# Performance work log

Measured on AMD Instinct MI355X. Metric: run time of the kernel, lower is better.

Reference implementation:

```python
import jax, jax.numpy as jnp
import numpy as np

HEADS = 8
DIM_HEAD = 64
SCALE = DIM_HEAD ** -0.5


def setup_inputs() -> dict:
    key = jax.random.key(0)
    ks = jax.random.split(key, 6)
    b, dim, h, w = 8, 512, 64, 64
    ctx_dim, n = 768, 256
    inner = HEADS * DIM_HEAD  # 512
    x = jax.random.normal(ks[0], (b, dim, h, w), jnp.float32)
    context = jax.random.normal(ks[1], (b, n, ctx_dim), jnp.float32)
    # 1x1 convs / linear reduced to [out, in] matrices
    Wq = jax.random.normal(ks[2], (inner, dim), jnp.float32) * 0.02
    Wkv = jax.random.normal(ks[3], (2 * inner, ctx_dim), jnp.float32) * 0.02
    Wout = jax.random.normal(ks[4], (dim, inner), jnp.float32) * 0.02
    bout = jnp.zeros((dim,), jnp.float32)
    return {"x": x, "context": context, "Wq": Wq, "Wkv": Wkv, "Wout": Wout, "bout": bout}


def reference(x, context, Wq, Wkv, Wout, bout):
    b, c, h, w = x.shape
    # to_q: 1x1 conv (no bias) == per-pixel channel matmul
    q = jnp.einsum('bcxy,ec->bexy', x, Wq)              # [b, inner, h, w]
    # rearrange 'b (h d) x y -> b h (x y) d'
    q = q.reshape(b, HEADS, DIM_HEAD, h * w).transpose(0, 1, 3, 2)
    # to_kv: Linear(context_dim -> 2*inner, no bias)
    kv = jnp.einsum('bnc,ec->bne', context, Wkv)        # [b, n, 2*inner]
    k, v = jnp.split(kv, 2, axis=-1)
    # rearrange 'b n (h d) -> b h n d'
    n = context.shape[1]
    k = k.reshape(b, n, HEADS, DIM_HEAD).transpose(0, 2, 1, 3)
    v = v.reshape(b, n, HEADS, DIM_HEAD).transpose(0, 2, 1, 3)
    sim = jnp.einsum('bhid,bhjd->bhij', q, k) * SCALE   # [b, h, hw, n]
    attn = jax.nn.softmax(sim, axis=-1)
    out = jnp.einsum('bhij,bhjd->bhid', attn, v)        # [b, h, hw, d]
    # rearrange 'b h (x y) d -> b (h d) x y'
    out = out.transpose(0, 1, 3, 2).reshape(b, HEADS * DIM_HEAD, h, w)
    # to_out: 1x1 conv with bias, plus residual
    out = jnp.einsum('bexy,ce->bcxy', out, Wout) + bout[None, :, None, None]
    return out + x
```

## Files before the change

kernel.cpp:

```cpp
#include <hip/hip_runtime.h>

typedef unsigned short u16;
typedef __bf16 bf16x8 __attribute__((ext_vector_type(8)));
typedef __bf16 bf16x4 __attribute__((ext_vector_type(4)));
typedef float f32x4 __attribute__((ext_vector_type(4)));

__device__ __forceinline__ u16 f2bf(float f) {
  __bf16 h = (__bf16)f;
  return *(u16*)&h;
}

__device__ __forceinline__ f32x4 mfma16(bf16x8 a, bf16x8 b, f32x4 c) {
  return __builtin_amdgcn_mfma_f32_16x16x32_bf16(a, b, c, 0, 0, 0);
}

__device__ __forceinline__ void async16(void* lds, const void* g) {
  __builtin_amdgcn_global_load_lds(
      (const __attribute__((address_space(1))) unsigned int*)g,
      (__attribute__((address_space(3))) unsigned int*)lds, 16, 0, 0);
}

#define QSCALE 0.18033688011112042f

__global__ __launch_bounds__(256) void prep_transpose(
    const float* __restrict__ x, const float* __restrict__ Wq,
    const float* __restrict__ Wkv, const float* __restrict__ Wout,
    const float* __restrict__ ctx, u16* __restrict__ xT,
    u16* __restrict__ Wq_b, u16* __restrict__ Wkv_b,
    u16* __restrict__ Wout_b, u16* __restrict__ ctx_b) {
  __shared__ float tile[64][65];
  int bx = blockIdx.x;
  if (bx < 1024) {
    const long NWQ = 512L * 512, NWKV = 1024L * 768, NWOUT = 512L * 512,
               NCTX = 2048L * 768;
    const long total = NWQ + NWKV + NWOUT + NCTX;
    long stride = 1024L * 256;
    for (long i = (long)bx * 256 + threadIdx.x; i < total; i += stride) {
      long j = i;
      if (j < NWQ) { Wq_b[j] = f2bf(Wq[j] * QSCALE); continue; }
      j -= NWQ;
      if (j < NWKV) { Wkv_b[j] = f2bf(Wkv[j]); continue; }
      j -= NWKV;
      if (j < NWOUT) { Wout_b[j] = f2bf(Wout[j]); continue; }
      j -= NWOUT;
      ctx_b[j] = f2bf(ctx[j]);
    }
    return;
  }
  bx -= 1024;
  const int p0 = (bx & 63) * 64, c0 = ((bx >> 6) & 7) * 64, b = bx >> 9;
  const int tx = threadIdx.x & 63, ty = threadIdx.x >> 6;
  const float* xb = x + (long)b * (512L * 4096);
  #pragma unroll
  for (int i = ty; i < 64; i += 4)
    tile[i][tx] = xb[(long)(c0 + i) * 4096 + p0 + tx];
  __syncthreads();
  u16* xTb = xT + (long)b * (4096L * 512);
  #pragma unroll
  for (int i = ty; i < 64; i += 4)
    xTb[(long)(p0 + i) * 512 + c0 + tx] = f2bf(tile[tx][i]);
}

__global__ __launch_bounds__(256) void transpose_v(const u16* __restrict__ kv,
                                                   u16* __restrict__ vT) {
  __shared__ u16 tile[64][65];
  const int b = blockIdx.z, e0 = blockIdx.x * 64, n0 = blockIdx.y * 64;
  const int tx = threadIdx.x & 63, ty = threadIdx.x >> 6;
  #pragma unroll
  for (int i = ty; i < 64; i += 4)
    tile[i][tx] = kv[(long)(b * 256 + n0 + i) * 1024 + 512 + e0 + tx];
  __syncthreads();
  #pragma unroll
  for (int i = ty; i < 64; i += 4)
    vT[(long)b * (512L * 256) + (long)(e0 + i) * 256 + n0 + tx] = tile[tx][i];
}

__global__ __launch_bounds__(512, 2) void gemm_qkv(
    const u16* __restrict__ xT, const u16* __restrict__ Wq,
    u16* __restrict__ q, const u16* __restrict__ ctxb,
    const u16* __restrict__ Wkv, u16* __restrict__ kvout) {
  __shared__ u16 ldsA[2][256 * 64];
  __shared__ u16 ldsB[2][256 * 64];
  const int t = threadIdx.x, wv = t >> 6, ln = t & 63;
  const int wr = wv >> 2, wc = wv & 3, fr = ln & 15, fq = ln >> 4;

  const int L = blockIdx.x;
  const u16 *A, *B;
  u16* C;
  int N, K, nk, m0, n0;
  if (L < 256) {
    const int z = L & 7, kq = L >> 3, pr = kq & 1, ld = kq >> 1;
    m0 = ld * 256;
    n0 = pr * 256;
    A = xT + (long)z * (4096L * 512);
    B = Wq;
    C = q + (long)z * (4096L * 512);
    N = 512; K = 512; nk = 8;
  } else {
    const int l2 = L - 256;
    m0 = (l2 & 7) * 256;
    n0 = (l2 >> 3) * 256;
    A = ctxb;
    B = Wkv;
    C = kvout;
    N = 1024; K = 768; nk = 12;
  }

  const u16* aSrc[4];
  const u16* bSrc[4];
  int lbase[4];
  #pragma unroll
  for (int i = 0; i < 4; i++) {
    int c = i * 512 + wv * 64 + ln;
    int row = c >> 3, slot = (c & 7) ^ (row & 7);
    aSrc[i] = A + (long)(m0 + row) * K + slot * 8;
    bSrc[i] = B + (long)(n0 + row) * K + slot * 8;
    lbase[i] = (i * 512 + wv * 64) * 8;
  }

  f32x4 acc[8][4] = {};
  int cur = 0;

  #pragma unroll
  for (int i = 0; i < 4; i++) {
    async16(&ldsA[0][lbase[i]], aSrc[i]);
    async16(&ldsB[0][lbase[i]], bSrc[i]);
  }

  for (int kt = 0; kt < nk; ++kt) {
    if (kt + 1 < nk) {
      const int ko = (kt + 1) * 64;
      #pragma unroll
      for (int i = 0; i < 4; i++) {
        async16(&ldsA[cur ^ 1][lbase[i]], aSrc[i] + ko);
        async16(&ldsB[cur ^ 1][lbase[i]], bSrc[i] + ko);
      }
      asm volatile("s_waitcnt vmcnt(8)" ::: "memory");
    } else {
      asm volatile("s_waitcnt vmcnt(0)" ::: "memory");
    }
    __builtin_amdgcn_s_barrier();
    __builtin_amdgcn_sched_barrier(0);

    const char* Ab = (const char*)ldsA[cur];
    const char* Bb = (const char*)ldsB[cur];
    #pragma unroll
    for (int kk = 0; kk < 2; ++kk) {
      bf16x8 a[8], b[4];
      #pragma unroll
      for (int mf = 0; mf < 8; ++mf) {
        int row = wr * 128 + mf * 16 + fr;
        a[mf] = *(const bf16x8*)(Ab + row * 128 +
                                 ((kk * 64 + fq * 16) ^ ((row & 7) << 4)));
      }
      #pragma unroll
      for (int nf = 0; nf < 4; ++nf) {
        int row = wc * 64 + nf * 16 + fr;
        b[nf] = *(const bf16x8*)(Bb + row * 128 +
                                 ((kk * 64 + fq * 16) ^ ((row & 7) << 4)));
      }
      __builtin_amdgcn_s_setprio(1);
      #pragma unroll
      for (int mf = 0; mf < 8; ++mf)
        #pragma unroll
        for (int nf = 0; nf < 4; ++nf)
          acc[mf][nf] = mfma16(a[mf], b[nf], acc[mf][nf]);
      __builtin_amdgcn_s_setprio(0);
    }

    __builtin_amdgcn_sched_barrier(0);
    __builtin_amdgcn_s_barrier();
    cur ^= 1;
  }

  #pragma unroll
  for (int mf = 0; mf < 8; ++mf)
    #pragma unroll
    for (int r = 0; r < 4; ++r) {
      int grow = m0 + wr * 128 + mf * 16 + fq * 4 + r;
      #pragma unroll
      for (int nf = 0; nf < 4; ++nf) {
        int gcol = n0 + wc * 64 + nf * 16 + fr;
        C[(long)grow * N + gcol] = f2bf(acc[mf][nf][r]);
      }
    }
}

__global__ __launch_bounds__(512, 2) void gemm_out(
    const u16* __restrict__ Wout, const u16* __restrict__ ao,
    float* __restrict__ out, const float* __restrict__ bias,
    const float* __restrict__ resid) {
  __shared__ u16 ldsA[2][256 * 64];
  __shared__ u16 ldsB[2][256 * 64];
  const int t = threadIdx.x, wv = t >> 6, ln = t & 63;
  const int wr = wv >> 2, wc = wv & 3, fr = ln & 15, fq = ln >> 4;

  const int L = blockIdx.x;
  const int z = L & 7, kq = L >> 3, pr = kq & 1, ld = kq >> 1;
  const int m0 = pr * 256;
  const int n0 = ld * 256;
  const int N = 4096, K = 512, nk = 8;

  const u16* A = Wout;
  const u16* B = ao + (long)z * (4096L * 512);

  const u16* aSrc[4];
  const u16* bSrc[4];
  int lbase[4];
  #pragma unroll
  for (int i = 0; i < 4; i++) {
    int c = i * 512 + wv * 64 + ln;
    int row = c >> 3, slot = (c & 7) ^ (row & 7);
    aSrc[i] = A + (long)(m0 + row) * K + slot * 8;
    bSrc[i] = B + (long)(n0 + row) * K + slot * 8;
    lbase[i] = (i * 512 + wv * 64) * 8;
  }

  f32x4 acc[8][4] = {};
  int cur = 0;

  #pragma unroll
  for (int i = 0; i < 4; i++) {
    async16(&ldsA[0][lbase[i]], aSrc[i]);
    async16(&ldsB[0][lbase[i]], bSrc[i]);
  }

  for (int kt = 0; kt < nk; ++kt) {
    if (kt + 1 < nk) {
      const int ko = (kt + 1) * 64;
      #pragma unroll
      for (int i = 0; i < 4; i++) {
        async16(&ldsA[cur ^ 1][lbase[i]], aSrc[i] + ko);
        async16(&ldsB[cur ^ 1][lbase[i]], bSrc[i] + ko);
      }
      asm volatile("s_waitcnt vmcnt(8)" ::: "memory");
    } else {
      asm volatile("s_waitcnt vmcnt(0)" ::: "memory");
    }
    __builtin_amdgcn_s_barrier();
    __builtin_amdgcn_sched_barrier(0);

    const char* Ab = (const char*)ldsA[cur];
    const char* Bb = (const char*)ldsB[cur];
    #pragma unroll
    for (int kk = 0; kk < 2; ++kk) {
      bf16x8 a[8], b[4];
      #pragma unroll
      for (int mf = 0; mf < 8; ++mf) {
        int row = wr * 128 + mf * 16 + fr;
        a[mf] = *(const bf16x8*)(Ab + row * 128 +
                                 ((kk * 64 + fq * 16) ^ ((row & 7) << 4)));
      }
      #pragma unroll
      for (int nf = 0; nf < 4; ++nf) {
        int row = wc * 64 + nf * 16 + fr;
        b[nf] = *(const bf16x8*)(Bb + row * 128 +
                                 ((kk * 64 + fq * 16) ^ ((row & 7) << 4)));
      }
      __builtin_amdgcn_s_setprio(1);
      #pragma unroll
      for (int mf = 0; mf < 8; ++mf)
        #pragma unroll
        for (int nf = 0; nf < 4; ++nf)
          acc[mf][nf] = mfma16(a[mf], b[nf], acc[mf][nf]);
      __builtin_amdgcn_s_setprio(0);
    }

    __builtin_amdgcn_sched_barrier(0);
    __builtin_amdgcn_s_barrier();
    cur ^= 1;
  }

  float* Cf = out + (long)z * (512L * 4096);
  const float* Rz = resid + (long)z * (512L * 4096);
  #pragma unroll
  for (int mf = 0; mf < 8; ++mf)
    #pragma unroll
    for (int r = 0; r < 4; ++r) {
      int grow = m0 + wr * 128 + mf * 16 + fq * 4 + r;
      float bv = bias[grow];
      #pragma unroll
      for (int nf = 0; nf < 4; ++nf) {
        int gcol = n0 + wc * 64 + nf * 16 + fr;
        long idx = (long)grow * N + gcol;
        Cf[idx] = acc[mf][nf][r] + bv + Rz[idx];
      }
    }
}

__global__ __launch_bounds__(512) void attn_kernel(
    const u16* __restrict__ q, const u16* __restrict__ kv,
    const u16* __restrict__ vT, u16* __restrict__ ao) {
  __shared__ u16 klds[256 * 64];
  __shared__ u16 vlds[64 * 256];
  __shared__ u16 plds[128 * 256];
  const int t = threadIdx.x, w = t >> 6, ln = t & 63;
  const int fr = ln & 15, fq = ln >> 4;
  const int p0 = blockIdx.x * 1024, h = blockIdx.y, b = blockIdx.z;

  const u16* kb = kv + (long)b * 256 * 1024 + h * 64;
  const u16* vb = vT + (long)b * (512L * 256) + (long)h * 64 * 256;

  #pragma unroll
  for (int i = 0; i < 4; ++i) {
    int cbase = i * 512 + w * 64;
    int chunk = cbase + ln;
    int row = chunk >> 3, slot = chunk & 7;
    async16(&klds[cbase * 8], kb + (long)row * 1024 + ((slot ^ (row & 7)) << 3));
  }
  #pragma unroll
  for (int i = 0; i < 4; ++i) {
    int cbase = i * 512 + w * 64;
    int chunk = cbase + ln;
    int row = chunk >> 5, slot = chunk & 31;
    async16(&vlds[cbase * 8], vb + (long)row * 256 + ((slot ^ (row & 7)) << 3));
  }
  __syncthreads();

  const char* kraw = (const char*)klds;
  const char* vraw = (const char*)vlds;
  char* praw = (char*)plds;
  const int prowL = w * 16 + fr;
  const int swz = (fr & 7) << 4;

  const u16* qbase = q + ((long)b * 4096 + p0 + w * 16 + fr) * 512 + h * 64;
  bf16x8 qf0 = *(const bf16x8*)&qbase[fq * 8];
  bf16x8 qf1 = *(const bf16x8*)&qbase[32 + fq * 8];

  for (int it = 0; it < 8; ++it) {
    f32x4 s[16] = {};
    __builtin_amdgcn_s_setprio(1);
    #pragma unroll
    for (int nb = 0; nb < 16; ++nb) {
      int n = nb * 16 + fr;
      bf16x8 kf0 = *(const bf16x8*)(kraw + n * 128 + ((fq * 16) ^ swz));
      bf16x8 kf1 = *(const bf16x8*)(kraw + n * 128 + ((64 + fq * 16) ^ swz));
      s[nb] = mfma16(kf0, qf0, s[nb]);
      s[nb] = mfma16(kf1, qf1, s[nb]);
    }
    __builtin_amdgcn_s_setprio(0);

    const u16* qn = qbase + (long)(((it + 1) & 7) * 128) * 512;
    bf16x8 qn0 = *(const bf16x8*)&qn[fq * 8];
    bf16x8 qn1 = *(const bf16x8*)&qn[32 + fq * 8];

    f32x4 mx = s[0];
    #pragma unroll
    for (int nb = 1; nb < 16; ++nb) {
      mx[0] = fmaxf(mx[0], s[nb][0]); mx[1] = fmaxf(mx[1], s[nb][1]);
      mx[2] = fmaxf(mx[2], s[nb][2]); mx[3] = fmaxf(mx[3], s[nb][3]);
    }
    float m = fmaxf(fmaxf(mx[0], mx[1]), fmaxf(mx[2], mx[3]));
    m = fmaxf(m, __shfl_xor(m, 16));
    m = fmaxf(m, __shfl_xor(m, 32));
    f32x4 sm = {0.f, 0.f, 0.f, 0.f};
    #pragma unroll
    for (int nb = 0; nb < 16; ++nb) {
      #pragma unroll
      for (int r = 0; r < 4; ++r)
        s[nb][r] = __builtin_amdgcn_exp2f(s[nb][r] - m);
      sm += s[nb];
    }
    float sum = (sm[0] + sm[1]) + (sm[2] + sm[3]);
    sum += __shfl_xor(sum, 16);
    sum += __shfl_xor(sum, 32);
    float inv = 1.0f / sum;

    #pragma unroll
    for (int nb = 0; nb < 16; ++nb) {
      bf16x4 pk;
      #pragma unroll
      for (int r = 0; r < 4; ++r) pk[r] = (__bf16)s[nb][r];
      *(bf16x4*)(praw + prowL * 512 + ((nb * 32 + fq * 8) ^ swz)) = pk;
    }
    asm volatile("s_waitcnt lgkmcnt(0)" ::: "memory");
    __builtin_amdgcn_sched_barrier(0);

    f32x4 o[4] = {};
    __builtin_amdgcn_s_setprio(1);
    #pragma unroll
    for (int kk2 = 0; kk2 < 8; ++kk2) {
      bf16x8 pf = *(const bf16x8*)(praw + prowL * 512 + ((kk2 * 64 + fq * 16) ^ swz));
      #pragma unroll
      for (int nfd = 0; nfd < 4; ++nfd) {
        bf16x8 vf = *(const bf16x8*)(vraw + (nfd * 16 + fr) * 512 +
                                     ((kk2 * 64 + fq * 16) ^ swz));
        o[nfd] = mfma16(vf, pf, o[nfd]);
      }
    }
    __builtin_amdgcn_s_setprio(0);

    u16* aob = ao + ((long)b * 4096 + p0 + it * 128 + w * 16 + fr) * 512 + h * 64;
    #pragma unroll
    for (int nfd = 0; nfd < 4; ++nfd) {
      bf16x4 ov;
      #pragma unroll
      for (int r = 0; r < 4; ++r) ov[r] = (__bf16)(o[nfd][r] * inv);
      *(bf16x4*)(aob + nfd * 16 + fq * 4) = ov;
    }
    qf0 = qn0;
    qf1 = qn1;
  }
}

extern "C" void kernel_launch(void* const* d_in, const int* in_sizes, int n_in,
                              void* d_out, int out_size, void* d_ws, size_t ws_size,
                              hipStream_t stream) {
  const float* x    = (const float*)d_in[0];
  const float* ctx  = (const float*)d_in[1];
  const float* Wq   = (const float*)d_in[2];
  const float* Wkv  = (const float*)d_in[3];
  const float* Wout = (const float*)d_in[4];
  const float* bout = (const float*)d_in[5];
  float* out = (float*)d_out;
  char* ws = (char*)d_ws;

  u16* xT     = (u16*)(ws);
  u16* q      = (u16*)(ws + 33554432);
  u16* kv     = (u16*)(ws + 67108864);
  u16* vT     = (u16*)(ws + 71303168);
  u16* Wq_b   = (u16*)(ws + 73400320);
  u16* Wkv_b  = (u16*)(ws + 73924608);
  u16* Wout_b = (u16*)(ws + 75497472);
  u16* ctx_b  = (u16*)(ws + 76021760);
  u16* ao     = xT;

  prep_transpose<<<dim3(5120), dim3(256), 0, stream>>>(
      x, Wq, Wkv, Wout, ctx, xT, Wq_b, Wkv_b, Wout_b, ctx_b);
  gemm_qkv<<<dim3(288), dim3(512), 0, stream>>>(
      xT, Wq_b, q, ctx_b, Wkv_b, kv);
  transpose_v<<<dim3(8, 4, 8), dim3(256), 0, stream>>>(kv, vT);
  attn_kernel<<<dim3(4, 8, 8), dim3(512), 0, stream>>>(q, kv, vT, ao);
  gemm_out<<<dim3(256), dim3(512), 0, stream>>>(
      Wout_b, ao, out, bout, x);
}
```

Measured before the change: 137.9 us.

## Fuse V transpose into attention, vectorize prep kernels, schedule KV GEMM tiles first

Removes the separate transpose_v kernel: the attention kernel now reads V rows directly from the kv buffer and scatters them transposed into swizzled LDS, saving a launch and a global round trip. The prep kernel's weight/context conversion and x transpose now use 16-byte loads and 8-wide bf16 stores instead of scalar accesses. The QKV GEMM block order is changed so the longer KV tiles are scheduled first. The in-LDS scatter uses 2-byte stores that may cause bank conflicts and synchronous loads in attention.

Result: faster. 124.9 us (-9.4%).

```diff
diff --git a/kernel.cpp b/kernel.cpp
--- a/kernel.cpp
+++ b/kernel.cpp
@@ -4,6 +4,8 @@
 typedef __bf16 bf16x8 __attribute__((ext_vector_type(8)));
 typedef __bf16 bf16x4 __attribute__((ext_vector_type(4)));
 typedef float f32x4 __attribute__((ext_vector_type(4)));
+typedef unsigned short u16x4 __attribute__((ext_vector_type(4)));
+typedef unsigned short u16x8 __attribute__((ext_vector_type(8)));
 
 __device__ __forceinline__ u16 f2bf(float f) {
   __bf16 h = (__bf16)f;
@@ -31,48 +33,49 @@
   __shared__ float tile[64][65];
   int bx = blockIdx.x;
   if (bx < 1024) {
-    const long NWQ = 512L * 512, NWKV = 1024L * 768, NWOUT = 512L * 512,
-               NCTX = 2048L * 768;
-    const long total = NWQ + NWKV + NWOUT + NCTX;
+    const long NWQ4 = 512L * 512 / 4, NWKV4 = 1024L * 768 / 4,
+               NWOUT4 = 512L * 512 / 4, NCTX4 = 2048L * 768 / 4;
+    const long total4 = NWQ4 + NWKV4 + NWOUT4 + NCTX4;
     long stride = 1024L * 256;
-    for (long i = (long)bx * 256 + threadIdx.x; i < total; i += stride) {
+    for (long i = (long)bx * 256 + threadIdx.x; i < total4; i += stride) {
       long j = i;
-      if (j < NWQ) { Wq_b[j] = f2bf(Wq[j] * QSCALE); continue; }
-      j -= NWQ;
-      if (j < NWKV) { Wkv_b[j] = f2bf(Wkv[j]); continue; }
-      j -= NWKV;
-      if (j < NWOUT) { Wout_b[j] = f2bf(Wout[j]); continue; }
-      j -= NWOUT;
-      ctx_b[j] = f2bf(ctx[j]);
+      const float* src;
+      u16* dst;
+      float sc = 1.0f;
+      if (j < NWQ4) { src = Wq; dst = Wq_b; sc = QSCALE; }
+      else if ((j -= NWQ4) < NWKV4) { src = Wkv; dst = Wkv_b; }
+      else if ((j -= NWKV4) < NWOUT4) { src = Wout; dst = Wout_b; }
+      else { j -= NWOUT4; src = ctx; dst = ctx_b; }
+      f32x4 v = *(const f32x4*)&src[j * 4];
+      u16x4 o;
+      #pragma unroll
+      for (int r = 0; r < 4; ++r) o[r] = f2bf(v[r] * sc);
+      *(u16x4*)&dst[j * 4] = o;
     }
     return;
   }
   bx -= 1024;
   const int p0 = (bx & 63) * 64, c0 = ((bx >> 6) & 7) * 64, b = bx >> 9;
-  const int tx = threadIdx.x & 63, ty = threadIdx.x >> 6;
   const float* xb = x + (long)b * (512L * 4096);
-  #pragma unroll
-  for (int i = ty; i < 64; i += 4)
-    tile[i][tx] = xb[(long)(c0 + i) * 4096 + p0 + tx];
+  const int ci0 = threadIdx.x >> 4, tx4 = threadIdx.x & 15;
+  #pragma unroll
+  for (int rep = 0; rep < 4; ++rep) {
+    int ci = ci0 + rep * 16;
+    f32x4 v = *(const f32x4*)&xb[(long)(c0 + ci) * 4096 + p0 + tx4 * 4];
+    #pragma unroll
+    for (int r = 0; r < 4; ++r) tile[ci][tx4 * 4 + r] = v[r];
+  }
   __syncthreads();
   u16* xTb = xT + (long)b * (4096L * 512);
-  #pragma unroll
-  for (int i = ty; i < 64; i += 4)
-    xTb[(long)(p0 + i) * 512 + c0 + tx] = f2bf(tile[tx][i]);
-}
-
-__global__ __launch_bounds__(256) void transpose_v(const u16* __restrict__ kv,
-                                                   u16* __restrict__ vT) {
-  __shared__ u16 tile[64][65];
-  const int b = blockIdx.z, e0 = blockIdx.x * 64, n0 = blockIdx.y * 64;
-  const int tx = threadIdx.x & 63, ty = threadIdx.x >> 6;
-  #pragma unroll
-  for (int i = ty; i < 64; i += 4)
-    tile[i][tx] = kv[(long)(b * 256 + n0 + i) * 1024 + 512 + e0 + tx];
-  __syncthreads();
-  #pragma unroll
-  for (int i = ty; i < 64; i += 4)
-    vT[(long)b * (512L * 256) + (long)(e0 + i) * 256 + n0 + tx] = tile[tx][i];
+  const int pi0 = threadIdx.x >> 3, cg = threadIdx.x & 7;
+  #pragma unroll
+  for (int rep = 0; rep < 2; ++rep) {
+    int pi = pi0 + rep * 32;
+    u16x8 o;
+    #pragma unroll
+    for (int j = 0; j < 8; ++j) o[j] = f2bf(tile[cg * 8 + j][pi]);
+    *(u16x8*)&xTb[(long)(p0 + pi) * 512 + c0 + cg * 8] = o;
+  }
 }
 
 __global__ __launch_bounds__(512, 2) void gemm_qkv(
@@ -88,22 +91,22 @@
   const u16 *A, *B;
   u16* C;
   int N, K, nk, m0, n0;
-  if (L < 256) {
-    const int z = L & 7, kq = L >> 3, pr = kq & 1, ld = kq >> 1;
+  if (L < 32) {
+    m0 = (L & 7) * 256;
+    n0 = (L >> 3) * 256;
+    A = ctxb;
+    B = Wkv;
+    C = kvout;
+    N = 1024; K = 768; nk = 12;
+  } else {
+    const int Lq = L - 32;
+    const int z = Lq & 7, kq = Lq >> 3, pr = kq & 1, ld = kq >> 1;
     m0 = ld * 256;
     n0 = pr * 256;
     A = xT + (long)z * (4096L * 512);
     B = Wq;
     C = q + (long)z * (4096L * 512);
     N = 512; K = 512; nk = 8;
-  } else {
-    const int l2 = L - 256;
-    m0 = (l2 & 7) * 256;
-    n0 = (l2 >> 3) * 256;
-    A = ctxb;
-    B = Wkv;
-    C = kvout;
-    N = 1024; K = 768; nk = 12;
   }
 
   const u16* aSrc[4];
@@ -290,7 +293,7 @@
 
 __global__ __launch_bounds__(512) void attn_kernel(
     const u16* __restrict__ q, const u16* __restrict__ kv,
-    const u16* __restrict__ vT, u16* __restrict__ ao) {
+    u16* __restrict__ ao) {
   __shared__ u16 klds[256 * 64];
   __shared__ u16 vlds[64 * 256];
   __shared__ u16 plds[128 * 256];
@@ -299,7 +302,6 @@
   const int p0 = blockIdx.x * 1024, h = blockIdx.y, b = blockIdx.z;
 
   const u16* kb = kv + (long)b * 256 * 1024 + h * 64;
-  const u16* vb = vT + (long)b * (512L * 256) + (long)h * 64 * 256;
 
   #pragma unroll
   for (int i = 0; i < 4; ++i) {
@@ -308,12 +310,21 @@
     int row = chunk >> 3, slot = chunk & 7;
     async16(&klds[cbase * 8], kb + (long)row * 1024 + ((slot ^ (row & 7)) << 3));
   }
-  #pragma unroll
-  for (int i = 0; i < 4; ++i) {
-    int cbase = i * 512 + w * 64;
-    int chunk = cbase + ln;
-    int row = chunk >> 5, slot = chunk & 31;
-    async16(&vlds[cbase * 8], vb + (long)row * 256 + ((slot ^ (row & 7)) << 3));
+  {
+    char* vw = (char*)vlds;
+    const u16* vsrc = kv + (long)b * 256 * 1024 + 512 + h * 64;
+    #pragma unroll
+    for (int it2 = 0; it2 < 4; ++it2) {
+      int id = it2 * 512 + t;
+      int n = id >> 3, dg = id & 7;
+      bf16x8 v8 = *(const bf16x8*)&vsrc[(long)n * 1024 + dg * 8];
+      #pragma unroll
+      for (int j = 0; j < 8; ++j) {
+        int jj = (j + (ln >> 3)) & 7;
+        int d = dg * 8 + jj;
+        *(u16*)(vw + ((d * 512 + n * 2) ^ ((d & 7) << 4))) = ((u16*)&v8)[jj];
+      }
+    }
   }
   __syncthreads();
 
@@ -418,7 +429,6 @@
   u16* xT     = (u16*)(ws);
   u16* q      = (u16*)(ws + 33554432);
   u16* kv     = (u16*)(ws + 67108864);
-  u16* vT     = (u16*)(ws + 71303168);
   u16* Wq_b   = (u16*)(ws + 73400320);
   u16* Wkv_b  = (u16*)(ws + 73924608);
   u16* Wout_b = (u16*)(ws + 75497472);
@@ -429,8 +439,7 @@
       x, Wq, Wkv, Wout, ctx, xT, Wq_b, Wkv_b, Wout_b, ctx_b);
   gemm_qkv<<<dim3(288), dim3(512), 0, stream>>>(
       xT, Wq_b, q, ctx_b, Wkv_b, kv);
-  transpose_v<<<dim3(8, 4, 8), dim3(256), 0, stream>>>(kv, vT);
-  attn_kernel<<<dim3(4, 8, 8), dim3(512), 0, stream>>>(q, kv, vT, ao);
+  attn_kernel<<<dim3(4, 8, 8), dim3(512), 0, stream>>>(q, kv, ao);
   gemm_out<<<dim3(256), dim3(512), 0, stream>>>(
       Wout_b, ao, out, bout, x);
 }
```
